# Kernel tuning notes

Hardware: AMD Instinct MI355X
Metric: run time of the kernel (lower is better)

## Reference

```python
import jax, jax.numpy as jnp
import numpy as np

N = 50000          # num nodes
E = 800000         # num edges (avg degree 16)
C_IN = 64          # input channels
TOWERS = 4
F_IN = C_IN // TOWERS       # 16 (divide_input=True)
OUT = 128
F_OUT = OUT // TOWERS       # 32
NUM_AGG = 4                 # mean, std, max, min
NUM_SC = 3                  # identity, amplification, attenuation
AVG_LOG_DEG = float(np.log(17.0))  # deg histogram: all nodes degree 16 -> log(16+1)


def setup_inputs() -> dict:
    key = jax.random.key(0)
    ks = jax.random.split(key, 10)
    nodes = jax.random.normal(ks[0], (N, C_IN), dtype=jnp.float32)
    senders = jax.random.randint(ks[1], (E,), 0, N)
    receivers = jax.random.randint(ks[2], (E,), 0, N)
    # per-tower pre-MLP: Linear(2*F_IN -> F_IN), pre_layers=1 (no activation)
    pre_w = jax.random.normal(ks[3], (TOWERS, 2 * F_IN, F_IN), dtype=jnp.float32) / np.sqrt(2 * F_IN)
    pre_b = jnp.zeros((TOWERS, F_IN), dtype=jnp.float32)
    # per-tower post-MLP: Linear(F_IN + F_IN*12 -> F_OUT), post_layers=1
    post_in = F_IN + F_IN * NUM_AGG * NUM_SC  # 208
    post_w = jax.random.normal(ks[4], (TOWERS, post_in, F_OUT), dtype=jnp.float32) / np.sqrt(post_in)
    post_b = jnp.zeros((TOWERS, F_OUT), dtype=jnp.float32)
    # final linear: TOWERS*F_OUT -> OUT
    lin_w = jax.random.normal(ks[5], (TOWERS * F_OUT, OUT), dtype=jnp.float32) / np.sqrt(TOWERS * F_OUT)
    lin_b = jnp.zeros((OUT,), dtype=jnp.float32)
    return {"nodes": nodes, "senders": senders, "receivers": receivers,
            "pre_w": pre_w, "pre_b": pre_b, "post_w": post_w, "post_b": post_b,
            "lin_w": lin_w, "lin_b": lin_b}


def reference(nodes, senders, receivers, pre_w, pre_b, post_w, post_b, lin_w, lin_b):
    # divide_input=True: split channels across towers -> [N, T, F_IN]
    x = nodes.reshape(N, TOWERS, F_IN)
    x_i = x[senders]                                  # [E, T, F_IN]
    x_j = x[receivers]                                # [E, T, F_IN]
    h = jnp.concatenate([x_i, x_j], axis=-1)          # [E, T, 2*F_IN]
    # per-tower pre-MLP (single linear), vectorized over towers
    msg = jnp.einsum('etf,tfo->eto', h, pre_w) + pre_b  # [E, T, F_IN]

    # degree-scaled multi-aggregator segment reduce over receivers
    count = jax.ops.segment_sum(jnp.ones((E,), dtype=msg.dtype), receivers, num_segments=N)  # [N]
    d = jnp.clip(count, 1.0, None)
    inv_d = (1.0 / d)[:, None, None]
    mean = jax.ops.segment_sum(msg, receivers, num_segments=N) * inv_d           # [N,T,F]
    mean_sq = jax.ops.segment_sum(msg * msg, receivers, num_segments=N) * inv_d
    std = jnp.sqrt(jax.nn.relu(mean_sq - mean * mean) + 1e-5)
    has_nb = (count > 0)[:, None, None]
    mx = jax.ops.segment_max(msg, receivers, num_segments=N)
    mx = jnp.where(has_nb, mx, 0.0)
    mn = -jax.ops.segment_max(-msg, receivers, num_segments=N)
    mn = jnp.where(has_nb, mn, 0.0)
    agg = jnp.concatenate([mean, std, mx, mn], axis=-1)  # [N, T, 4*F_IN]

    # scalers: identity, amplification, attenuation (degree clamped to >= 1)
    log_d = jnp.log(d + 1.0)[:, None, None]
    amp = log_d / AVG_LOG_DEG
    att = AVG_LOG_DEG / log_d
    scaled = jnp.concatenate([agg, agg * amp, agg * att], axis=-1)  # [N, T, 12*F_IN]

    out = jnp.concatenate([x, scaled], axis=-1)                     # [N, T, 13*F_IN]
    outs = jnp.einsum('ntf,tfo->nto', out, post_w) + post_b         # [N, T, F_OUT]
    flat = outs.reshape(N, TOWERS * F_OUT)                          # [N, 128]
    return flat @ lin_w + lin_b                                     # [N, OUT]
```

## Files before the change

### kernel.cpp

```cpp
#include <hip/hip_runtime.h>

#define AVG_LOG_DEG 2.8332133440562162f
#define CAP 64

typedef __attribute__((ext_vector_type(8))) short short8;
typedef __attribute__((ext_vector_type(4))) float f32x4;

static __device__ __forceinline__ float bl(unsigned u) { return __uint_as_float(u << 16); }
static __device__ __forceinline__ float bh(unsigned u) { return __uint_as_float(u & 0xffff0000u); }
static __device__ __forceinline__ unsigned short f2b(float f) {
    unsigned u = __float_as_uint(f);
    return (unsigned short)((u + 0x7fffu + ((u >> 16) & 1u)) >> 16);
}
static __device__ __forceinline__ unsigned pk(unsigned short lo, unsigned short hi) {
    return (unsigned)lo | ((unsigned)hi << 16);
}


__global__ void k_init(int* __restrict__ cursor, int n) {
    int i = blockIdx.x * 256 + threadIdx.x;
    if (i < n) cursor[i] = 0;
}

__global__ __launch_bounds__(256) void k_scatter2(
    const int* __restrict__ send, const int* __restrict__ recv,
    int* __restrict__ cursor, int* __restrict__ slots,
    int e, int nps)
{
    int slice = blockIdx.x & 7;
    int chunk = blockIdx.x >> 3;
    int base = chunk * 2048;
    int lo = slice * nps;
    #pragma unroll
    for (int it = 0; it < 8; ++it) {
        int i = base + it * 256 + threadIdx.x;
        if (i < e) {
            int r = recv[i];
            if ((unsigned)(r - lo) < (unsigned)nps) {
                int p = atomicAdd(&cursor[r], 1);
                if (p < CAP) slots[(size_t)r * CAP + p] = send[i];
            }
        }
    }
}


__global__ void k_prew(const float* __restrict__ post_w, const float* __restrict__ lin_w,
                       unsigned short* __restrict__ postT, unsigned short* __restrict__ linT) {
    int i = blockIdx.x * 256 + threadIdx.x;
    if (i < 28672) {
        int t = i / (32 * 224);
        int r = i % (32 * 224);
        int nn = r / 224;
        int k = r % 224;
        float wv;
        if (k < 192)      wv = post_w[((size_t)t * 208 + 16 + k) * 32 + nn];
        else if (k < 208) wv = post_w[((size_t)t * 208 + (k - 192)) * 32 + nn];
        else              wv = 0.f;
        postT[i] = f2b(wv);
    }
    int j = i - 28672;
    if (j >= 0 && j < 16384) {
        int nn = j >> 7, k = j & 127;
        linT[j] = f2b(lin_w[k * 128 + nn]);
    }
}


__global__ __launch_bounds__(256) void k_pre(
    const float* __restrict__ nodes,
    const float* __restrict__ pre_w,
    float* __restrict__ Y, int n)
{
    int lane = threadIdx.x & 63;
    int node = blockIdx.x * 4 + (threadIdx.x >> 6);
    if (node >= n) return;
    int t = lane >> 4, f = lane & 15;
    float w[16];
    #pragma unroll
    for (int k = 0; k < 16; ++k)
        w[k] = pre_w[(t * 32 + k) * 16 + f];
    const float4* xp = reinterpret_cast<const float4*>(nodes + (size_t)node * 64 + t * 16);
    float4 x0 = xp[0], x1 = xp[1], x2 = xp[2], x3 = xp[3];
    float xs[16] = {x0.x, x0.y, x0.z, x0.w, x1.x, x1.y, x1.z, x1.w,
                    x2.x, x2.y, x2.z, x2.w, x3.x, x3.y, x3.z, x3.w};
    float y = 0.f;
    #pragma unroll
    for (int k = 0; k < 16; ++k)
        y = fmaf(xs[k], w[k], y);
    Y[(size_t)node * 64 + lane] = y;
}


__global__ __launch_bounds__(256) void k_agg(
    const float* __restrict__ nodes,
    const float* __restrict__ pre_w,
    const float* __restrict__ pre_b,
    const int* __restrict__ cursor,
    const int* __restrict__ slots, const float* __restrict__ Y,
    unsigned short* __restrict__ aggh, int n)
{
    int lane = threadIdx.x & 63;
    int node = blockIdx.x * 4 + (threadIdx.x >> 6);
    if (node >= n) return;
    int t = lane >> 4, f = lane & 15;

    float w[16];
    #pragma unroll
    for (int k = 0; k < 16; ++k)
        w[k] = pre_w[(t * 32 + 16 + k) * 16 + f];
    const float4* xp = reinterpret_cast<const float4*>(nodes + (size_t)node * 64 + t * 16);
    float4 x0 = xp[0], x1 = xp[1], x2 = xp[2], x3 = xp[3];
    float xs[16] = {x0.x, x0.y, x0.z, x0.w, x1.x, x1.y, x1.z, x1.w,
                    x2.x, x2.y, x2.z, x2.w, x3.x, x3.y, x3.z, x3.w};
    float hjw = pre_b[t * 16 + f];
    #pragma unroll
    for (int k = 0; k < 16; ++k)
        hjw = fmaf(xs[k], w[k], hjw);

    int d = min(cursor[node], CAP);
    const int* sl = slots + (size_t)node * CAP;
    const float* Yp = Y + lane;
    float s = 0.f, s2 = 0.f, mx = -INFINITY, mn = INFINITY;
    int e = 0;
    for (; e + 4 <= d; e += 4) {
        int i0 = sl[e], i1 = sl[e + 1], i2 = sl[e + 2], i3 = sl[e + 3];
        float m0 = Yp[(size_t)i0 * 64] + hjw;
        float m1 = Yp[(size_t)i1 * 64] + hjw;
        float m2 = Yp[(size_t)i2 * 64] + hjw;
        float m3 = Yp[(size_t)i3 * 64] + hjw;
        s += (m0 + m1) + (m2 + m3);
        s2 = fmaf(m0, m0, s2); s2 = fmaf(m1, m1, s2);
        s2 = fmaf(m2, m2, s2); s2 = fmaf(m3, m3, s2);
        mx = fmaxf(mx, fmaxf(fmaxf(m0, m1), fmaxf(m2, m3)));
        mn = fminf(mn, fminf(fminf(m0, m1), fminf(m2, m3)));
    }
    for (; e < d; ++e) {
        int i0 = sl[e];
        float m0 = Yp[(size_t)i0 * 64] + hjw;
        s += m0;
        s2 = fmaf(m0, m0, s2);
        mx = fmaxf(mx, m0);
        mn = fminf(mn, m0);
    }

    float dc = fmaxf((float)d, 1.f);
    float inv = 1.f / dc;
    float mean = s * inv;
    float var = fmaf(-mean, mean, s2 * inv);
    float sd = sqrtf(fmaxf(var, 0.f) + 1e-5f);
    if (d == 0) { mx = 0.f; mn = 0.f; }

    unsigned short* ag = aggh + (size_t)node * 256 + t * 64 + f;
    ag[0]  = f2b(mean);
    ag[16] = f2b(sd);
    ag[32] = f2b(mx);
    ag[48] = f2b(mn);
}


__global__ __launch_bounds__(256) void k_post(
    const float* __restrict__ nodes,
    const unsigned short* __restrict__ aggh,
    const int* __restrict__ deg,
    const unsigned short* __restrict__ postT,
    const unsigned short* __restrict__ linT,
    const float* __restrict__ post_b,
    const float* __restrict__ lin_b,
    float* __restrict__ out, int n)
{
    __shared__ unsigned short sV[32 * 256];
    __shared__ unsigned short sFlat[32 * 128];
    __shared__ float sAmp[32], sAtt[32];

    int tid = threadIdx.x;
    int n0 = blockIdx.x * 32;

    if (tid < 32) {
        int g = min(n0 + tid, n - 1);
        float dc = fmaxf((float)min(deg[g], CAP), 1.f);
        float ld = logf(dc + 1.f);
        sAmp[tid] = ld * (1.f / AVG_LOG_DEG);
        sAtt[tid] = AVG_LOG_DEG / ld;
    }
    __syncthreads();

    int w = tid >> 6, lane = tid & 63;
    int quad = lane >> 4, mr = lane & 15;
    int mstrip = w & 1, nhalf = w >> 1;
    int nn = tid >> 3, j8 = tid & 7;
    int sw = nn & 7;
    int gn = min(n0 + nn, n - 1);
    int rsw = mr & 7;

    for (int t = 0; t < 4; ++t) {
        short8 bfr[7];
        {
            const unsigned short* bp = postT + (size_t)(t * 32 + nhalf * 16 + mr) * 224 + quad * 8;
            #pragma unroll
            for (int kk = 0; kk < 7; ++kk)
                bfr[kk] = *reinterpret_cast<const short8*>(bp + kk * 32);
        }

        {
            float amp = sAmp[nn], att = sAtt[nn];
            unsigned short* row = &sV[nn * 256];
            uint4 a = *reinterpret_cast<const uint4*>(aggh + (size_t)gn * 256 + t * 64 + j8 * 8);
            *reinterpret_cast<uint4*>(row + (j8 ^ sw) * 8) = a;
            unsigned uu[4] = {a.x, a.y, a.z, a.w};
            unsigned short pa[8], pb[8];
            #pragma unroll
            for (int q = 0; q < 4; ++q) {
                float lo = bl(uu[q]), hi = bh(uu[q]);
                pa[2*q]   = f2b(lo * amp); pa[2*q+1] = f2b(hi * amp);
                pb[2*q]   = f2b(lo * att); pb[2*q+1] = f2b(hi * att);
            }
            uint4 wa, wb;
            wa.x = pk(pa[0], pa[1]); wa.y = pk(pa[2], pa[3]);
            wa.z = pk(pa[4], pa[5]); wa.w = pk(pa[6], pa[7]);
            wb.x = pk(pb[0], pb[1]); wb.y = pk(pb[2], pb[3]);
            wb.z = pk(pb[4], pb[5]); wb.w = pk(pb[6], pb[7]);
            *reinterpret_cast<uint4*>(row + (8  + (j8 ^ sw)) * 8) = wa;
            *reinterpret_cast<uint4*>(row + (16 + (j8 ^ sw)) * 8) = wb;
            uint4 xw; xw.x = 0; xw.y = 0; xw.z = 0; xw.w = 0;
            if (j8 < 2) {
                const float4* xp = reinterpret_cast<const float4*>(nodes + (size_t)gn * 64 + t * 16 + j8 * 8);
                float4 xa = xp[0], xb = xp[1];
                xw.x = pk(f2b(xa.x), f2b(xa.y)); xw.y = pk(f2b(xa.z), f2b(xa.w));
                xw.z = pk(f2b(xb.x), f2b(xb.y)); xw.w = pk(f2b(xb.z), f2b(xb.w));
            }
            *reinterpret_cast<uint4*>(row + (24 + (j8 ^ sw)) * 8) = xw;
        }
        __syncthreads();

        f32x4 acc = {0.f, 0.f, 0.f, 0.f};
        const unsigned short* av0 = &sV[(mstrip * 16 + mr) * 256];
        #pragma unroll
        for (int kk = 0; kk < 7; ++kk) {
            int c = kk * 4 + quad;
            int pc = (c & ~7) | ((c & 7) ^ rsw);
            short8 avv = *reinterpret_cast<const short8*>(av0 + pc * 8);
            acc = __builtin_amdgcn_mfma_f32_16x16x32_bf16(avv, bfr[kk], acc, 0, 0, 0);
        }

        int col = t * 32 + nhalf * 16 + mr;
        float pbv = post_b[col];
        int cc = col >> 3, co = col & 7;
        #pragma unroll
        for (int i = 0; i < 4; ++i) {
            int rowf = mstrip * 16 + quad * 4 + i;
            int pc = (cc & ~7) | ((cc & 7) ^ (rowf & 7));
            sFlat[rowf * 128 + pc * 8 + co] = f2b(acc[i] + pbv);
        }
        __syncthreads();
    }

    f32x4 facc[4];
    #pragma unroll
    for (int nt = 0; nt < 4; ++nt) { facc[nt].x = 0.f; facc[nt].y = 0.f; facc[nt].z = 0.f; facc[nt].w = 0.f; }

    const unsigned short* af0 = &sFlat[(mstrip * 16 + mr) * 128];
    #pragma unroll
    for (int kk = 0; kk < 4; ++kk) {
        int c = kk * 4 + quad;
        int pc = (c & ~7) | ((c & 7) ^ rsw);
        short8 avv = *reinterpret_cast<const short8*>(af0 + pc * 8);
        #pragma unroll
        for (int nt = 0; nt < 4; ++nt) {
            short8 bv = *reinterpret_cast<const short8*>(
                linT + (size_t)(nhalf * 64 + nt * 16 + mr) * 128 + kk * 32 + quad * 8);
            facc[nt] = __builtin_amdgcn_mfma_f32_16x16x32_bf16(avv, bv, facc[nt], 0, 0, 0);
        }
    }

    #pragma unroll
    for (int nt = 0; nt < 4; ++nt) {
        int col = nhalf * 64 + nt * 16 + mr;
        float lb = lin_b[col];
        #pragma unroll
        for (int i = 0; i < 4; ++i) {
            int node = n0 + mstrip * 16 + quad * 4 + i;
            if (node < n) out[(size_t)node * 128 + col] = facc[nt][i] + lb;
        }
    }
}

extern "C" void kernel_launch(void* const* d_in, const int* in_sizes, int n_in,
                              void* d_out, int out_size, void* d_ws, size_t ws_size,
                              hipStream_t stream)
{
    const float* nodes  = (const float*)d_in[0];
    const int*   send   = (const int*)d_in[1];
    const int*   recv   = (const int*)d_in[2];
    const float* pre_w  = (const float*)d_in[3];
    const float* pre_b  = (const float*)d_in[4];
    const float* post_w = (const float*)d_in[5];
    const float* post_b = (const float*)d_in[6];
    const float* lin_w  = (const float*)d_in[7];
    const float* lin_b  = (const float*)d_in[8];
    float* out = (float*)d_out;

    int N = in_sizes[0] / 64;
    int E = in_sizes[1];
    int Npad = (N + 255) & ~255;

    int* cursor = (int*)d_ws;
    int* slots  = cursor + Npad;
    float* Y    = (float*)(slots + (size_t)Npad * CAP);
    unsigned short* aggh  = (unsigned short*)(Y + (size_t)Npad * 64);
    unsigned short* postT = aggh + (size_t)Npad * 256;
    unsigned short* linT  = postT + 28672;

    int nbN = (N + 255) / 256;
    int nps = (N + 7) / 8;
    int nbS = 8 * ((E + 2047) / 2048);

    k_prew    <<<176, 256, 0, stream>>>(post_w, lin_w, postT, linT);
    k_init    <<<nbN, 256, 0, stream>>>(cursor, N);
    k_scatter2<<<nbS, 256, 0, stream>>>(send, recv, cursor, slots, E, nps);
    k_pre     <<<(N + 3) / 4, 256, 0, stream>>>(nodes, pre_w, Y, N);
    k_agg     <<<(N + 3) / 4, 256, 0, stream>>>(nodes, pre_w, pre_b, cursor, slots, Y, aggh, N);
    k_post    <<<(N + 31) / 32, 256, 0, stream>>>(nodes, aggh, cursor, postT, linT,
                                                  post_b, lin_b, out, N);
}
```

Measured before the change: 213.7 us.

## Merge setup kernels, batch neighbor gathers via readlane, prefetch post-MLP operands

Merges the pre-projection, weight-transpose and cursor-init kernels into one launch to cut launch count. In the aggregation kernel, each wave loads its whole slot list in one coalesced read and broadcasts indices with readlane, so 16 neighbor gathers can be issued before any arithmetic. The post kernel prefetches all aggregate and node inputs plus double-buffered weight fragments into registers ahead of the tower loop, and gains an occupancy hint. The cost is higher register pressure and a padded 16-wide tail loop that issues redundant loads.

```diff
diff --git a/kernel.cpp b/kernel.cpp
--- a/kernel.cpp
+++ b/kernel.cpp
@@ -17,10 +17,56 @@
 }
 
 
-__global__ void k_init(int* __restrict__ cursor, int n) {
-    int i = blockIdx.x * 256 + threadIdx.x;
-    if (i < n) cursor[i] = 0;
-}
+__global__ __launch_bounds__(256) void k_setup(
+    const float* __restrict__ nodes, const float* __restrict__ pre_w,
+    const float* __restrict__ post_w, const float* __restrict__ lin_w,
+    float* __restrict__ Y, unsigned short* __restrict__ postT,
+    unsigned short* __restrict__ linT, int* __restrict__ cursor,
+    int n, int A, int nbN)
+{
+    int b = blockIdx.x;
+    if (b < A) {
+        int lane = threadIdx.x & 63;
+        int node = b * 4 + (threadIdx.x >> 6);
+        if (node >= n) return;
+        int t = lane >> 4, f = lane & 15;
+        float w[16];
+        #pragma unroll
+        for (int k = 0; k < 16; ++k)
+            w[k] = pre_w[(t * 32 + k) * 16 + f];
+        const float4* xp = reinterpret_cast<const float4*>(nodes + (size_t)node * 64 + t * 16);
+        float4 x0 = xp[0], x1 = xp[1], x2 = xp[2], x3 = xp[3];
+        float xs[16] = {x0.x, x0.y, x0.z, x0.w, x1.x, x1.y, x1.z, x1.w,
+                        x2.x, x2.y, x2.z, x2.w, x3.x, x3.y, x3.z, x3.w};
+        float y = 0.f;
+        #pragma unroll
+        for (int k = 0; k < 16; ++k)
+            y = fmaf(xs[k], w[k], y);
+        Y[(size_t)node * 64 + lane] = y;
+    } else if (b < A + 176) {
+        int i = (b - A) * 256 + threadIdx.x;
+        if (i < 28672) {
+            int t = i / (32 * 224);
+            int r = i % (32 * 224);
+            int nn = r / 224;
+            int k = r % 224;
+            float wv;
+            if (k < 192)      wv = post_w[((size_t)t * 208 + 16 + k) * 32 + nn];
+            else if (k < 208) wv = post_w[((size_t)t * 208 + (k - 192)) * 32 + nn];
+            else              wv = 0.f;
+            postT[i] = f2b(wv);
+        }
+        int j = i - 28672;
+        if (j >= 0 && j < 16384) {
+            int nn = j >> 7, k = j & 127;
+            linT[j] = f2b(lin_w[k * 128 + nn]);
+        }
+    } else {
+        int i = (b - A - 176) * 256 + threadIdx.x;
+        if (i < n) cursor[i] = 0;
+    }
+}
+
 
 __global__ __launch_bounds__(256) void k_scatter2(
     const int* __restrict__ send, const int* __restrict__ recv,
@@ -45,53 +91,6 @@
 }
 
 
-__global__ void k_prew(const float* __restrict__ post_w, const float* __restrict__ lin_w,
-                       unsigned short* __restrict__ postT, unsigned short* __restrict__ linT) {
-    int i = blockIdx.x * 256 + threadIdx.x;
-    if (i < 28672) {
-        int t = i / (32 * 224);
-        int r = i % (32 * 224);
-        int nn = r / 224;
-        int k = r % 224;
-        float wv;
-        if (k < 192)      wv = post_w[((size_t)t * 208 + 16 + k) * 32 + nn];
-        else if (k < 208) wv = post_w[((size_t)t * 208 + (k - 192)) * 32 + nn];
-        else              wv = 0.f;
-        postT[i] = f2b(wv);
-    }
-    int j = i - 28672;
-    if (j >= 0 && j < 16384) {
-        int nn = j >> 7, k = j & 127;
-        linT[j] = f2b(lin_w[k * 128 + nn]);
-    }
-}
-
-
-__global__ __launch_bounds__(256) void k_pre(
-    const float* __restrict__ nodes,
-    const float* __restrict__ pre_w,
-    float* __restrict__ Y, int n)
-{
-    int lane = threadIdx.x & 63;
-    int node = blockIdx.x * 4 + (threadIdx.x >> 6);
-    if (node >= n) return;
-    int t = lane >> 4, f = lane & 15;
-    float w[16];
-    #pragma unroll
-    for (int k = 0; k < 16; ++k)
-        w[k] = pre_w[(t * 32 + k) * 16 + f];
-    const float4* xp = reinterpret_cast<const float4*>(nodes + (size_t)node * 64 + t * 16);
-    float4 x0 = xp[0], x1 = xp[1], x2 = xp[2], x3 = xp[3];
-    float xs[16] = {x0.x, x0.y, x0.z, x0.w, x1.x, x1.y, x1.z, x1.w,
-                    x2.x, x2.y, x2.z, x2.w, x3.x, x3.y, x3.z, x3.w};
-    float y = 0.f;
-    #pragma unroll
-    for (int k = 0; k < 16; ++k)
-        y = fmaf(xs[k], w[k], y);
-    Y[(size_t)node * 64 + lane] = y;
-}
-
-
 __global__ __launch_bounds__(256) void k_agg(
     const float* __restrict__ nodes,
     const float* __restrict__ pre_w,
@@ -105,6 +104,8 @@
     if (node >= n) return;
     int t = lane >> 4, f = lane & 15;
 
+    int idxv = slots[(size_t)node * CAP + lane];
+
     float w[16];
     #pragma unroll
     for (int k = 0; k < 16; ++k)
@@ -119,29 +120,44 @@
         hjw = fmaf(xs[k], w[k], hjw);
 
     int d = min(cursor[node], CAP);
-    const int* sl = slots + (size_t)node * CAP;
-    const float* Yp = Y + lane;
+    const float* Yl = Y + lane;
+
     float s = 0.f, s2 = 0.f, mx = -INFINITY, mn = INFINITY;
     int e = 0;
-    for (; e + 4 <= d; e += 4) {
-        int i0 = sl[e], i1 = sl[e + 1], i2 = sl[e + 2], i3 = sl[e + 3];
-        float m0 = Yp[(size_t)i0 * 64] + hjw;
-        float m1 = Yp[(size_t)i1 * 64] + hjw;
-        float m2 = Yp[(size_t)i2 * 64] + hjw;
-        float m3 = Yp[(size_t)i3 * 64] + hjw;
-        s += (m0 + m1) + (m2 + m3);
-        s2 = fmaf(m0, m0, s2); s2 = fmaf(m1, m1, s2);
-        s2 = fmaf(m2, m2, s2); s2 = fmaf(m3, m3, s2);
-        mx = fmaxf(mx, fmaxf(fmaxf(m0, m1), fmaxf(m2, m3)));
-        mn = fminf(mn, fminf(fminf(m0, m1), fminf(m2, m3)));
-    }
-    for (; e < d; ++e) {
-        int i0 = sl[e];
-        float m0 = Yp[(size_t)i0 * 64] + hjw;
-        s += m0;
-        s2 = fmaf(m0, m0, s2);
-        mx = fmaxf(mx, m0);
-        mn = fminf(mn, m0);
+    for (; e + 16 <= d; e += 16) {
+        float v[16];
+        #pragma unroll
+        for (int q = 0; q < 16; ++q) {
+            int si = __builtin_amdgcn_readlane(idxv, e + q);
+            v[q] = Yl[(size_t)si * 64];
+        }
+        #pragma unroll
+        for (int q = 0; q < 16; ++q) {
+            float m = v[q] + hjw;
+            s += m;
+            s2 = fmaf(m, m, s2);
+            mx = fmaxf(mx, m);
+            mn = fminf(mn, m);
+        }
+    }
+    int rem = d - e;
+    if (rem > 0) {
+        float v[16];
+        #pragma unroll
+        for (int q = 0; q < 16; ++q) {
+            int si = __builtin_amdgcn_readlane(idxv, min(e + q, d - 1));
+            v[q] = Yl[(size_t)si * 64];
+        }
+        #pragma unroll
+        for (int q = 0; q < 16; ++q) {
+            if (q < rem) {
+                float m = v[q] + hjw;
+                s += m;
+                s2 = fmaf(m, m, s2);
+                mx = fmaxf(mx, m);
+                mn = fminf(mn, m);
+            }
+        }
     }
 
     float dc = fmaxf((float)d, 1.f);
@@ -159,7 +175,7 @@
 }
 
 
-__global__ __launch_bounds__(256) void k_post(
+__global__ __launch_bounds__(256, 3) void k_post(
     const float* __restrict__ nodes,
     const unsigned short* __restrict__ aggh,
     const int* __restrict__ deg,
@@ -183,7 +199,6 @@
         sAmp[tid] = ld * (1.f / AVG_LOG_DEG);
         sAtt[tid] = AVG_LOG_DEG / ld;
     }
-    __syncthreads();
 
     int w = tid >> 6, lane = tid & 63;
     int quad = lane >> 4, mr = lane & 15;
@@ -193,27 +208,47 @@
     int gn = min(n0 + nn, n - 1);
     int rsw = mr & 7;
 
+    uint4 pa4[4];
+    #pragma unroll
+    for (int t = 0; t < 4; ++t)
+        pa4[t] = *reinterpret_cast<const uint4*>(aggh + (size_t)gn * 256 + t * 64 + j8 * 8);
+
+    uint4 xw4[4];
+    #pragma unroll
+    for (int t = 0; t < 4; ++t) { xw4[t].x = 0; xw4[t].y = 0; xw4[t].z = 0; xw4[t].w = 0; }
+    if (j8 < 2) {
+        #pragma unroll
+        for (int t = 0; t < 4; ++t) {
+            const float4* xp = reinterpret_cast<const float4*>(nodes + (size_t)gn * 64 + t * 16 + j8 * 8);
+            float4 xa = xp[0], xb = xp[1];
+            xw4[t].x = pk(f2b(xa.x), f2b(xa.y)); xw4[t].y = pk(f2b(xa.z), f2b(xa.w));
+            xw4[t].z = pk(f2b(xb.x), f2b(xb.y)); xw4[t].w = pk(f2b(xb.z), f2b(xb.w));
+        }
+    }
+
+    const unsigned short* bbase = postT + (size_t)(nhalf * 16 + mr) * 224 + quad * 8;
+    short8 bA[7], bB[7];
+    #pragma unroll
+    for (int kk = 0; kk < 7; ++kk) bA[kk] = *reinterpret_cast<const short8*>(bbase + kk * 32);
+    #pragma unroll
+    for (int kk = 0; kk < 7; ++kk) bB[kk] = *reinterpret_cast<const short8*>(bbase + 32 * 224 + kk * 32);
+
+    __syncthreads();
+    float ampv = sAmp[nn], attv = sAtt[nn];
+
+    #pragma unroll
     for (int t = 0; t < 4; ++t) {
-        short8 bfr[7];
         {
-            const unsigned short* bp = postT + (size_t)(t * 32 + nhalf * 16 + mr) * 224 + quad * 8;
-            #pragma unroll
-            for (int kk = 0; kk < 7; ++kk)
-                bfr[kk] = *reinterpret_cast<const short8*>(bp + kk * 32);
-        }
-
-        {
-            float amp = sAmp[nn], att = sAtt[nn];
             unsigned short* row = &sV[nn * 256];
-            uint4 a = *reinterpret_cast<const uint4*>(aggh + (size_t)gn * 256 + t * 64 + j8 * 8);
+            uint4 a = pa4[t];
             *reinterpret_cast<uint4*>(row + (j8 ^ sw) * 8) = a;
             unsigned uu[4] = {a.x, a.y, a.z, a.w};
             unsigned short pa[8], pb[8];
             #pragma unroll
             for (int q = 0; q < 4; ++q) {
                 float lo = bl(uu[q]), hi = bh(uu[q]);
-                pa[2*q]   = f2b(lo * amp); pa[2*q+1] = f2b(hi * amp);
-                pb[2*q]   = f2b(lo * att); pb[2*q+1] = f2b(hi * att);
+                pa[2*q]   = f2b(lo * ampv); pa[2*q+1] = f2b(hi * ampv);
+                pb[2*q]   = f2b(lo * attv); pb[2*q+1] = f2b(hi * attv);
             }
             uint4 wa, wb;
             wa.x = pk(pa[0], pa[1]); wa.y = pk(pa[2], pa[3]);
@@ -222,14 +257,7 @@
             wb.z = pk(pb[4], pb[5]); wb.w = pk(pb[6], pb[7]);
             *reinterpret_cast<uint4*>(row + (8  + (j8 ^ sw)) * 8) = wa;
             *reinterpret_cast<uint4*>(row + (16 + (j8 ^ sw)) * 8) = wb;
-            uint4 xw; xw.x = 0; xw.y = 0; xw.z = 0; xw.w = 0;
-            if (j8 < 2) {
-                const float4* xp = reinterpret_cast<const float4*>(nodes + (size_t)gn * 64 + t * 16 + j8 * 8);
-                float4 xa = xp[0], xb = xp[1];
-                xw.x = pk(f2b(xa.x), f2b(xa.y)); xw.y = pk(f2b(xa.z), f2b(xa.w));
-                xw.z = pk(f2b(xb.x), f2b(xb.y)); xw.w = pk(f2b(xb.z), f2b(xb.w));
-            }
-            *reinterpret_cast<uint4*>(row + (24 + (j8 ^ sw)) * 8) = xw;
+            *reinterpret_cast<uint4*>(row + (24 + (j8 ^ sw)) * 8) = xw4[t];
         }
         __syncthreads();
 
@@ -240,7 +268,18 @@
             int c = kk * 4 + quad;
             int pc = (c & ~7) | ((c & 7) ^ rsw);
             short8 avv = *reinterpret_cast<const short8*>(av0 + pc * 8);
-            acc = __builtin_amdgcn_mfma_f32_16x16x32_bf16(avv, bfr[kk], acc, 0, 0, 0);
+            if (t & 1) acc = __builtin_amdgcn_mfma_f32_16x16x32_bf16(avv, bB[kk], acc, 0, 0, 0);
+            else       acc = __builtin_amdgcn_mfma_f32_16x16x32_bf16(avv, bA[kk], acc, 0, 0, 0);
+        }
+
+        if (t == 0) {
+            #pragma unroll
+            for (int kk = 0; kk < 7; ++kk)
+                bA[kk] = *reinterpret_cast<const short8*>(bbase + 2 * 32 * 224 + kk * 32);
+        } else if (t == 1) {
+            #pragma unroll
+            for (int kk = 0; kk < 7; ++kk)
+                bB[kk] = *reinterpret_cast<const short8*>(bbase + 3 * 32 * 224 + kk * 32);
         }
 
         int col = t * 32 + nhalf * 16 + mr;
@@ -312,13 +351,13 @@
     unsigned short* linT  = postT + 28672;
 
     int nbN = (N + 255) / 256;
+    int A = (N + 3) / 4;
     int nps = (N + 7) / 8;
     int nbS = 8 * ((E + 2047) / 2048);
 
-    k_prew    <<<176, 256, 0, stream>>>(post_w, lin_w, postT, linT);
-    k_init    <<<nbN, 256, 0, stream>>>(cursor, N);
+    k_setup   <<<A + 176 + nbN, 256, 0, stream>>>(nodes, pre_w, post_w, lin_w,
+                                                  Y, postT, linT, cursor, N, A, nbN);
     k_scatter2<<<nbS, 256, 0, stream>>>(send, recv, cursor, slots, E, nps);
-    k_pre     <<<(N + 3) / 4, 256, 0, stream>>>(nodes, pre_w, Y, N);
     k_agg     <<<(N + 3) / 4, 256, 0, stream>>>(nodes, pre_w, pre_b, cursor, slots, Y, aggh, N);
     k_post    <<<(N + 31) / 32, 256, 0, stream>>>(nodes, aggh, cursor, postT, linT,
                                                   post_b, lin_b, out, N);
```

Result: faster. 201.8 us (-5.6%).
